# Kernel tuning notes

Measured on AMD Instinct MI355X. Metric: run time of the kernel, lower is better.

The kernel has to match this reference:

```python
import jax, jax.numpy as jnp
import numpy as np

D_MODEL = 1024
NUM_HEADS = 16
D_K = D_MODEL // NUM_HEADS


def setup_inputs() -> dict:
    key = jax.random.key(0)
    ks = jax.random.split(key, 11)
    s = 1.0 / np.sqrt(D_MODEL)
    return {
        "Q": jax.random.normal(ks[0], (2, 2048, D_MODEL), jnp.float32),
        "K": jax.random.normal(ks[1], (2, 2048, D_MODEL), jnp.float32),
        "V": jax.random.normal(ks[2], (2, 2048, D_MODEL), jnp.float32),
        "W_Q": jax.random.uniform(ks[3], (D_MODEL, D_MODEL), jnp.float32, -s, s),
        "b_Q": jax.random.uniform(ks[4], (D_MODEL,), jnp.float32, -s, s),
        "W_K": jax.random.uniform(ks[5], (D_K, D_MODEL), jnp.float32, -s, s),
        "b_K": jax.random.uniform(ks[6], (D_K,), jnp.float32, -s, s),
        "W_V": jax.random.uniform(ks[7], (D_K, D_MODEL), jnp.float32, -s, s),
        "b_V": jax.random.uniform(ks[8], (D_K,), jnp.float32, -s, s),
        "W_O": jax.random.uniform(ks[9], (D_MODEL, D_MODEL), jnp.float32, -s, s),
        "b_O": jax.random.uniform(ks[10], (D_MODEL,), jnp.float32, -s, s),
    }


def reference(Q, K, V, W_Q, b_Q, W_K, b_K, W_V, b_V, W_O, b_O):
    B, S, _ = Q.shape
    # Q projection -> [B, H, S, d_k]
    q = (Q @ W_Q.T + b_Q).reshape(B, S, NUM_HEADS, D_K).transpose(0, 2, 1, 3)
    # shared single-head K/V -> [B, S, d_k] (broadcast across heads)
    k = K @ W_K.T + b_K
    v = V @ W_V.T + b_V
    scale = 1.0 / jnp.sqrt(jnp.asarray(D_K, q.dtype))
    scores = jnp.einsum('bhqd,bkd->bhqk', q, k) * scale  # [B,H,S,S]
    attn = jax.nn.softmax(scores, axis=-1)
    out = jnp.einsum('bhqk,bkd->bhqd', attn, v)  # [B,H,S,d_k]
    out = out.transpose(0, 2, 1, 3).reshape(B, S, D_MODEL)
    return out @ W_O.T + b_O
```

## Files before the change

### kernel.cpp

```cpp
#include <hip/hip_runtime.h>
#include <hip/hip_bf16.h>
#include <math.h>

#define D_MODEL 1024
#define NUM_HEADS 16
#define DK 64
#define BATCH 2
#define SEQ 2048
#define MROWS (BATCH * SEQ)

#define QSCALE (0.125f * 1.4426950408889634f)

typedef __attribute__((ext_vector_type(8))) short bf16x8;
typedef __attribute__((ext_vector_type(4))) float f32x4;

static __device__ __forceinline__ short f2bf(float f) {
    __hip_bfloat16 h = __float2bfloat16(f);
    union { __hip_bfloat16 h; short s; } c; c.h = h; return c.s;
}

static __device__ __forceinline__ unsigned pkbf2(float a, float b) {
    __hip_bfloat162 h = __float22bfloat162_rn(make_float2(a, b));
    union { __hip_bfloat162 h; unsigned u; } c; c.h = h; return c.u;
}

static __device__ __forceinline__ void gload16(const void* g, void* l) {
    __builtin_amdgcn_global_load_lds(
        (const __attribute__((address_space(1))) unsigned int*)g,
        (__attribute__((address_space(3))) unsigned int*)l, 16, 0, 0);
}

__global__ __launch_bounds__(256) void cvt6(
    const float* __restrict__ q, const float* __restrict__ k,
    const float* __restrict__ v, const float* __restrict__ wq,
    const float* __restrict__ wo, const float* __restrict__ wk,
    const float* __restrict__ wv,
    short* __restrict__ qo, short* __restrict__ ko, short* __restrict__ vo,
    short* __restrict__ wqo, short* __restrict__ woo, short* __restrict__ wko,
    short* __restrict__ wvo)
{
    const int NB = (MROWS * D_MODEL) / 8;
    const int NW = (D_MODEL * D_MODEL) / 8;
    const int NS = (DK * D_MODEL) / 8;
    const int total = 3 * NB + 2 * NW + 2 * NS;
    for (int g = blockIdx.x * 256 + threadIdx.x; g < total; g += gridDim.x * 256) {
        const float* s; short* d; int x = g;
        if (x < NB)            { s = q;  d = qo;  }
        else if ((x -= NB) < NB) { s = k;  d = ko;  }
        else if ((x -= NB) < NB) { s = v;  d = vo;  }
        else if ((x -= NB) < NW) { s = wq; d = wqo; }
        else if ((x -= NW) < NW) { s = wo; d = woo; }
        else if ((x -= NW) < NS) { s = wk; d = wko; }
        else                     { x -= NS; s = wv; d = wvo; }
        float4 a = ((const float4*)s)[x * 2];
        float4 b = ((const float4*)s)[x * 2 + 1];
        uint4 hv;
        hv.x = pkbf2(a.x, a.y); hv.y = pkbf2(a.z, a.w);
        hv.z = pkbf2(b.x, b.y); hv.w = pkbf2(b.z, b.w);
        ((uint4*)d)[x] = hv;
    }
}

template<int MODE, int BM, int BN>
__global__ __launch_bounds__(256) void gemm97(
    const short* __restrict__ A, const short* __restrict__ W,
    const float* __restrict__ bias, void* __restrict__ Cp,
    const short* __restrict__ A2, const short* __restrict__ W2,
    const float* __restrict__ bias2, void* __restrict__ Cp2,
    int M, int N, int K, float outmult)
{
    constexpr int MI = BM / 32;
    constexpr int NI = BN / 32;
    constexpr int ACH = BM / 32;
    constexpr int WCH = BN / 32;
    __shared__ short As[BM * 64];
    __shared__ short Ws[BN * 64];

    int sel = 0;
    if (MODE == 2) {
        sel = blockIdx.y;
        if (sel) { A = A2; W = W2; bias = bias2; Cp = Cp2; }
    }
    const int bm = blockIdx.x * BM;
    const int bn = (MODE == 2) ? 0 : blockIdx.y * BN;
    const int tid = threadIdx.x;
    const int l = tid & 63, w = tid >> 6;
    const int lr = l & 15, lg = l >> 4;
    const int wm = (w >> 1) * (BM / 2), wn = (w & 1) * (BN / 2);

    f32x4 acc[MI][NI];
    #pragma unroll
    for (int mi = 0; mi < MI; mi++)
        #pragma unroll
        for (int ni = 0; ni < NI; ni++)
            acc[mi][ni] = (f32x4){0.f, 0.f, 0.f, 0.f};

    const int srow = l >> 3;
    const int scol = (l & 7) * 8;

    for (int k0 = 0; k0 < K; k0 += 64) {
        __syncthreads();
        #pragma unroll
        for (int i = 0; i < ACH; i++) {
            int c = w * ACH + i;
            gload16(A + (size_t)(bm + 8 * c + srow) * K + k0 + scol, As + c * 512);
        }
        #pragma unroll
        for (int i = 0; i < WCH; i++) {
            int c = w * WCH + i;
            gload16(W + (size_t)(bn + 8 * c + srow) * K + k0 + scol, Ws + c * 512);
        }
        __syncthreads();
        #pragma unroll
        for (int ks = 0; ks < 2; ks++) {
            bf16x8 af[MI], bf[NI];
            #pragma unroll
            for (int mi = 0; mi < MI; mi++)
                af[mi] = *(const bf16x8*)&As[(wm + mi * 16 + lr) * 64 + ks * 32 + 8 * lg];
            #pragma unroll
            for (int ni = 0; ni < NI; ni++)
                bf[ni] = *(const bf16x8*)&Ws[(wn + ni * 16 + lr) * 64 + ks * 32 + 8 * lg];
            #pragma unroll
            for (int mi = 0; mi < MI; mi++)
                #pragma unroll
                for (int ni = 0; ni < NI; ni++)
                    acc[mi][ni] = __builtin_amdgcn_mfma_f32_16x16x32_bf16(
                        af[mi], bf[ni], acc[mi][ni], 0, 0, 0);
        }
    }

    #pragma unroll
    for (int ni = 0; ni < NI; ni++) {
        int col = bn + wn + ni * 16 + lr;
        float bv = bias[col];
        #pragma unroll
        for (int mi = 0; mi < MI; mi++) {
            #pragma unroll
            for (int r = 0; r < 4; r++) {
                int row = bm + wm + mi * 16 + lg * 4 + r;
                float val = (acc[mi][ni][r] + bv) * outmult;
                if (MODE == 0) {
                    ((short*)Cp)[(size_t)row * N + col] = f2bf(val);
                } else if (MODE == 1) {
                    ((float*)Cp)[(size_t)row * N + col] = val;
                } else {
                    if (sel == 0) {
                        ((short*)Cp)[(size_t)row * DK + col] = f2bf(val);
                    } else {
                        int bi = row >> 11, si = row & (SEQ - 1);
                        int s6 = si & 63;
                        int sperm = (si & ~63) | (s6 & 32) |
                                    (((s6 >> 3) & 1) << 4) | (((s6 >> 2) & 1) << 3) |
                                    (((s6 >> 4) & 1) << 2) | (s6 & 3);
                        ((short*)Cp)[((size_t)bi * DK + col) * SEQ + sperm] = f2bf(val);
                    }
                }
            }
        }
    }
}

__global__ __launch_bounds__(128, 2) void mqa_attn_lds(
    const short* __restrict__ qb, const short* __restrict__ kb,
    const short* __restrict__ vt, short* __restrict__ ob)
{
    __shared__ char KsB[2][64 * 128];
    __shared__ char VsB[2][64 * 128];
    const int h = blockIdx.y, b = blockIdx.z;
    const int tid = threadIdx.x;
    const int l = tid & 63, w = tid >> 6;
    const int lr = l & 15, lg = l >> 4;
    const int q0 = blockIdx.x * 64 + w * 32;

    bf16x8 qf[2][2];
    #pragma unroll
    for (int qt = 0; qt < 2; qt++)
        #pragma unroll
        for (int kk = 0; kk < 2; kk++)
            qf[qt][kk] = *(const bf16x8*)(
                qb + (size_t)(b * SEQ + q0 + qt * 16 + lr) * D_MODEL + h * DK + kk * 32 + 8 * lg);

    int srow[4], scol[4];
    #pragma unroll
    for (int i = 0; i < 4; i++) {
        int s = i * 128 + w * 64 + l;
        srow[i] = s >> 3;
        int cb = (s & 7) * 16;
        scol[i] = (cb ^ ((srow[i] & 7) << 4)) >> 1;
    }

    f32x4 o[4][2];
    #pragma unroll
    for (int dt = 0; dt < 4; dt++)
        #pragma unroll
        for (int qt = 0; qt < 2; qt++)
            o[dt][qt] = (f32x4){0.f, 0.f, 0.f, 0.f};
    float m_i[2] = {-1e30f, -1e30f};
    float l_l[2] = {0.f, 0.f};

    #pragma unroll
    for (int i = 0; i < 4; i++) {
        gload16(kb + (size_t)(b * SEQ + 0 + srow[i]) * DK + scol[i],
                KsB[0] + (i * 128 + w * 64) * 16);
        gload16(vt + (size_t)(b * DK + srow[i]) * SEQ + 0 + scol[i],
                VsB[0] + (i * 128 + w * 64) * 16);
    }

    for (int t = 0; t < SEQ / 64; t++) {
        const int cur = t & 1;
        const int kt = t * 64;
        __syncthreads();
        if (t + 1 < SEQ / 64) {
            const int ktn = kt + 64;
            #pragma unroll
            for (int i = 0; i < 4; i++) {
                gload16(kb + (size_t)(b * SEQ + ktn + srow[i]) * DK + scol[i],
                        KsB[cur ^ 1] + (i * 128 + w * 64) * 16);
                gload16(vt + (size_t)(b * DK + srow[i]) * SEQ + ktn + scol[i],
                        VsB[cur ^ 1] + (i * 128 + w * 64) * 16);
            }
        }
        const char* Kc = KsB[cur];
        const char* Vc = VsB[cur];

        f32x4 s[2][4];
        #pragma unroll
        for (int qt = 0; qt < 2; qt++)
            #pragma unroll
            for (int j = 0; j < 4; j++) s[qt][j] = (f32x4){0.f, 0.f, 0.f, 0.f};
        #pragma unroll
        for (int kk = 0; kk < 2; kk++) {
            bf16x8 kf[4];
            #pragma unroll
            for (int j = 0; j < 4; j++) {
                int row = j * 16 + lr;
                kf[j] = *(const bf16x8*)(Kc + row * 128 + ((kk * 64 + 16 * lg) ^ ((row & 7) << 4)));
            }
            __builtin_amdgcn_s_setprio(1);
            #pragma unroll
            for (int qt = 0; qt < 2; qt++)
                #pragma unroll
                for (int j = 0; j < 4; j++)
                    s[qt][j] = __builtin_amdgcn_mfma_f32_16x16x32_bf16(
                        kf[j], qf[qt][kk], s[qt][j], 0, 0, 0);
            __builtin_amdgcn_s_setprio(0);
        }

        bf16x8 vf[2][4];
        #pragma unroll
        for (int kk = 0; kk < 2; kk++)
            #pragma unroll
            for (int dt = 0; dt < 4; dt++) {
                int row = dt * 16 + lr;
                vf[kk][dt] = *(const bf16x8*)(Vc + row * 128 + ((kk * 64 + 16 * lg) ^ ((row & 7) << 4)));
            }

        union { unsigned u[4]; bf16x8 v; } pku[2][2];
        #pragma unroll
        for (int qt = 0; qt < 2; qt++) {
            float mA = fmaxf(fmaxf(s[qt][0][0], s[qt][0][1]), s[qt][0][2]);
            float mB = fmaxf(fmaxf(s[qt][0][3], s[qt][1][0]), s[qt][1][1]);
            float mC = fmaxf(fmaxf(s[qt][1][2], s[qt][1][3]), s[qt][2][0]);
            float mD = fmaxf(fmaxf(s[qt][2][1], s[qt][2][2]), s[qt][2][3]);
            float mE = fmaxf(fmaxf(s[qt][3][0], s[qt][3][1]), s[qt][3][2]);
            float mx = fmaxf(fmaxf(fmaxf(mA, mB), mC),
                             fmaxf(fmaxf(mD, mE), s[qt][3][3]));

            if (__any(mx > m_i[qt] + 8.0f)) {
                float mxf = fmaxf(mx, __shfl_xor(mx, 16));
                mxf = fmaxf(mxf, __shfl_xor(mxf, 32));
                float mn = fmaxf(m_i[qt], mxf);
                float corr = __builtin_amdgcn_exp2f(m_i[qt] - mn);
                m_i[qt] = mn;
                l_l[qt] *= corr;
                #pragma unroll
                for (int dt = 0; dt < 4; dt++)
                    o[dt][qt] *= corr;
            }
            const float mnv = m_i[qt];

            float p[4][4];
            float rs = 0.f;
            #pragma unroll
            for (int j = 0; j < 4; j++) {
                p[j][0] = __builtin_amdgcn_exp2f(s[qt][j][0] - mnv);
                p[j][1] = __builtin_amdgcn_exp2f(s[qt][j][1] - mnv);
                p[j][2] = __builtin_amdgcn_exp2f(s[qt][j][2] - mnv);
                p[j][3] = __builtin_amdgcn_exp2f(s[qt][j][3] - mnv);
                rs += (p[j][0] + p[j][1]) + (p[j][2] + p[j][3]);
            }
            l_l[qt] += rs;

            pku[qt][0].u[0] = pkbf2(p[0][0], p[0][1]);
            pku[qt][0].u[1] = pkbf2(p[0][2], p[0][3]);
            pku[qt][0].u[2] = pkbf2(p[1][0], p[1][1]);
            pku[qt][0].u[3] = pkbf2(p[1][2], p[1][3]);
            pku[qt][1].u[0] = pkbf2(p[2][0], p[2][1]);
            pku[qt][1].u[1] = pkbf2(p[2][2], p[2][3]);
            pku[qt][1].u[2] = pkbf2(p[3][0], p[3][1]);
            pku[qt][1].u[3] = pkbf2(p[3][2], p[3][3]);
        }

        __builtin_amdgcn_s_setprio(1);
        #pragma unroll
        for (int kk = 0; kk < 2; kk++)
            #pragma unroll
            for (int dt = 0; dt < 4; dt++)
                #pragma unroll
                for (int qt = 0; qt < 2; qt++)
                    o[dt][qt] = __builtin_amdgcn_mfma_f32_16x16x32_bf16(
                        vf[kk][dt], pku[qt][kk].v, o[dt][qt], 0, 0, 0);
        __builtin_amdgcn_s_setprio(0);
    }

    #pragma unroll
    for (int qt = 0; qt < 2; qt++) {
        float lt = l_l[qt];
        lt += __shfl_xor(lt, 16);
        lt += __shfl_xor(lt, 32);
        float inv = 1.0f / lt;
        size_t grow = (size_t)(b * SEQ + q0 + qt * 16 + lr);
        #pragma unroll
        for (int dt = 0; dt < 4; dt++) {
            uint2 pk;
            pk.x = pkbf2(o[dt][qt][0] * inv, o[dt][qt][1] * inv);
            pk.y = pkbf2(o[dt][qt][2] * inv, o[dt][qt][3] * inv);
            *(uint2*)(ob + grow * D_MODEL + h * DK + dt * 16 + lg * 4) = pk;
        }
    }
}

extern "C" void kernel_launch(void* const* d_in, const int* in_sizes, int n_in,
                              void* d_out, int out_size, void* d_ws, size_t ws_size,
                              hipStream_t stream) {
    const float* Q   = (const float*)d_in[0];
    const float* K   = (const float*)d_in[1];
    const float* V   = (const float*)d_in[2];
    const float* W_Q = (const float*)d_in[3];
    const float* b_Q = (const float*)d_in[4];
    const float* W_K = (const float*)d_in[5];
    const float* b_K = (const float*)d_in[6];
    const float* W_V = (const float*)d_in[7];
    const float* b_V = (const float*)d_in[8];
    const float* W_O = (const float*)d_in[9];
    const float* b_O = (const float*)d_in[10];
    float* out = (float*)d_out;

    short* Qb  = (short*)d_ws;
    short* Kb  = Qb  + (size_t)MROWS * D_MODEL;
    short* Vb  = Kb  + (size_t)MROWS * D_MODEL;
    short* WQb = Vb  + (size_t)MROWS * D_MODEL;
    short* WKb = WQb + (size_t)D_MODEL * D_MODEL;
    short* WVb = WKb + (size_t)DK * D_MODEL;
    short* WOb = WVb + (size_t)DK * D_MODEL;
    short* qb  = WOb + (size_t)D_MODEL * D_MODEL;
    short* kb  = qb  + (size_t)MROWS * D_MODEL;
    short* vt  = kb  + (size_t)MROWS * DK;
    short* aws = vt  + (size_t)MROWS * DK;

    cvt6<<<2048, 256, 0, stream>>>(Q, K, V, W_Q, W_O, W_K, W_V,
                                   Qb, Kb, Vb, WQb, WOb, WKb, WVb);

    gemm97<0, 64, 128><<<dim3(MROWS / 64, D_MODEL / 128), 256, 0, stream>>>(
        Qb, WQb, b_Q, qb, nullptr, nullptr, nullptr, nullptr,
        MROWS, D_MODEL, D_MODEL, QSCALE);
    gemm97<2, 64, 64><<<dim3(MROWS / 64, 2), 256, 0, stream>>>(
        Kb, WKb, b_K, kb, Vb, WVb, b_V, vt, MROWS, DK, D_MODEL, 1.0f);
    mqa_attn_lds<<<dim3(SEQ / 64, NUM_HEADS, BATCH), 128, 0, stream>>>(
        qb, kb, vt, aws);
    gemm97<1, 64, 128><<<dim3(MROWS / 64, D_MODEL / 128), 256, 0, stream>>>(
        aws, WOb, b_O, out, nullptr, nullptr, nullptr, nullptr,
        MROWS, D_MODEL, D_MODEL, 1.0f);
}
```

Before: 131.3 us.

## Split KV tiles across wave pairs to overlap QK^T with softmax/PV, merge partials

The attention kernel now uses 256 threads: two wave pairs share each 64-query block, and each pair owns alternating KV tiles. In a given iteration one pair runs the QK^T MFMAs while the other runs softmax and PV on its earlier tile, so matrix and exponential work from different waves can overlap. At the end the two partial softmax states (max, sum, output) are merged through LDS. This adds an extra barrier per tile and an LDS combine step, and each wave keeps its score accumulators live across iterations, which raises register pressure.

Result: slower. 139.6 us (+6.4%).

```diff
diff --git a/kernel.cpp b/kernel.cpp
--- a/kernel.cpp
+++ b/kernel.cpp
@@ -160,17 +160,18 @@
     }
 }
 
-__global__ __launch_bounds__(128, 2) void mqa_attn_lds(
+__global__ __launch_bounds__(256, 4) void mqa_attn_pipe(
     const short* __restrict__ qb, const short* __restrict__ kb,
     const short* __restrict__ vt, short* __restrict__ ob)
 {
     __shared__ char KsB[2][64 * 128];
     __shared__ char VsB[2][64 * 128];
-    const int h = blockIdx.y, b = blockIdx.z;
+    const int hd = blockIdx.y, b = blockIdx.z;
     const int tid = threadIdx.x;
     const int l = tid & 63, w = tid >> 6;
+    const int qg = w >> 1, kp = w & 1;
     const int lr = l & 15, lg = l >> 4;
-    const int q0 = blockIdx.x * 64 + w * 32;
+    const int q0 = blockIdx.x * 64 + qg * 32;
 
     bf16x8 qf[2][2];
     #pragma unroll
@@ -178,12 +179,12 @@
         #pragma unroll
         for (int kk = 0; kk < 2; kk++)
             qf[qt][kk] = *(const bf16x8*)(
-                qb + (size_t)(b * SEQ + q0 + qt * 16 + lr) * D_MODEL + h * DK + kk * 32 + 8 * lg);
-
-    int srow[4], scol[4];
-    #pragma unroll
-    for (int i = 0; i < 4; i++) {
-        int s = i * 128 + w * 64 + l;
+                qb + (size_t)(b * SEQ + q0 + qt * 16 + lr) * D_MODEL + hd * DK + kk * 32 + 8 * lg);
+
+    int srow[2], scol[2];
+    #pragma unroll
+    for (int i = 0; i < 2; i++) {
+        int s = i * 256 + tid;
         srow[i] = s >> 3;
         int cb = (s & 7) * 16;
         scol[i] = (cb ^ ((srow[i] & 7) << 4)) >> 1;
@@ -197,75 +198,30 @@
             o[dt][qt] = (f32x4){0.f, 0.f, 0.f, 0.f};
     float m_i[2] = {-1e30f, -1e30f};
     float l_l[2] = {0.f, 0.f};
-
-    #pragma unroll
-    for (int i = 0; i < 4; i++) {
-        gload16(kb + (size_t)(b * SEQ + 0 + srow[i]) * DK + scol[i],
-                KsB[0] + (i * 128 + w * 64) * 16);
-        gload16(vt + (size_t)(b * DK + srow[i]) * SEQ + 0 + scol[i],
-                VsB[0] + (i * 128 + w * 64) * 16);
-    }
-
-    for (int t = 0; t < SEQ / 64; t++) {
-        const int cur = t & 1;
-        const int kt = t * 64;
-        __syncthreads();
-        if (t + 1 < SEQ / 64) {
-            const int ktn = kt + 64;
-            #pragma unroll
-            for (int i = 0; i < 4; i++) {
-                gload16(kb + (size_t)(b * SEQ + ktn + srow[i]) * DK + scol[i],
-                        KsB[cur ^ 1] + (i * 128 + w * 64) * 16);
-                gload16(vt + (size_t)(b * DK + srow[i]) * SEQ + ktn + scol[i],
-                        VsB[cur ^ 1] + (i * 128 + w * 64) * 16);
-            }
-        }
-        const char* Kc = KsB[cur];
-        const char* Vc = VsB[cur];
-
-        f32x4 s[2][4];
-        #pragma unroll
-        for (int qt = 0; qt < 2; qt++)
-            #pragma unroll
-            for (int j = 0; j < 4; j++) s[qt][j] = (f32x4){0.f, 0.f, 0.f, 0.f};
-        #pragma unroll
-        for (int kk = 0; kk < 2; kk++) {
-            bf16x8 kf[4];
-            #pragma unroll
-            for (int j = 0; j < 4; j++) {
-                int row = j * 16 + lr;
-                kf[j] = *(const bf16x8*)(Kc + row * 128 + ((kk * 64 + 16 * lg) ^ ((row & 7) << 4)));
-            }
-            __builtin_amdgcn_s_setprio(1);
-            #pragma unroll
-            for (int qt = 0; qt < 2; qt++)
-                #pragma unroll
-                for (int j = 0; j < 4; j++)
-                    s[qt][j] = __builtin_amdgcn_mfma_f32_16x16x32_bf16(
-                        kf[j], qf[qt][kk], s[qt][j], 0, 0, 0);
-            __builtin_amdgcn_s_setprio(0);
-        }
-
-        bf16x8 vf[2][4];
-        #pragma unroll
-        for (int kk = 0; kk < 2; kk++)
-            #pragma unroll
-            for (int dt = 0; dt < 4; dt++) {
-                int row = dt * 16 + lr;
-                vf[kk][dt] = *(const bf16x8*)(Vc + row * 128 + ((kk * 64 + 16 * lg) ^ ((row & 7) << 4)));
-            }
-
-        union { unsigned u[4]; bf16x8 v; } pku[2][2];
+    f32x4 sS[2][4];
+
+    #pragma unroll
+    for (int i = 0; i < 2; i++) {
+        gload16(kb + (size_t)(b * SEQ + srow[i]) * DK + scol[i],
+                KsB[0] + (i * 256 + tid) * 16);
+        gload16(vt + (size_t)(b * DK + srow[i]) * SEQ + scol[i],
+                VsB[0] + (i * 256 + tid) * 16);
+    }
+
+    const char* Kc = KsB[kp];
+    const char* Vc = VsB[kp];
+
+    auto finishTile = [&]() {
+        union PKU { unsigned u[4]; bf16x8 v; } pku[2][2];
         #pragma unroll
         for (int qt = 0; qt < 2; qt++) {
-            float mA = fmaxf(fmaxf(s[qt][0][0], s[qt][0][1]), s[qt][0][2]);
-            float mB = fmaxf(fmaxf(s[qt][0][3], s[qt][1][0]), s[qt][1][1]);
-            float mC = fmaxf(fmaxf(s[qt][1][2], s[qt][1][3]), s[qt][2][0]);
-            float mD = fmaxf(fmaxf(s[qt][2][1], s[qt][2][2]), s[qt][2][3]);
-            float mE = fmaxf(fmaxf(s[qt][3][0], s[qt][3][1]), s[qt][3][2]);
+            float mA = fmaxf(fmaxf(sS[qt][0][0], sS[qt][0][1]), sS[qt][0][2]);
+            float mB = fmaxf(fmaxf(sS[qt][0][3], sS[qt][1][0]), sS[qt][1][1]);
+            float mC = fmaxf(fmaxf(sS[qt][1][2], sS[qt][1][3]), sS[qt][2][0]);
+            float mD = fmaxf(fmaxf(sS[qt][2][1], sS[qt][2][2]), sS[qt][2][3]);
+            float mE = fmaxf(fmaxf(sS[qt][3][0], sS[qt][3][1]), sS[qt][3][2]);
             float mx = fmaxf(fmaxf(fmaxf(mA, mB), mC),
-                             fmaxf(fmaxf(mD, mE), s[qt][3][3]));
-
+                             fmaxf(fmaxf(mD, mE), sS[qt][3][3]));
             if (__any(mx > m_i[qt] + 8.0f)) {
                 float mxf = fmaxf(mx, __shfl_xor(mx, 16));
                 mxf = fmaxf(mxf, __shfl_xor(mxf, 32));
@@ -278,19 +234,17 @@
                     o[dt][qt] *= corr;
             }
             const float mnv = m_i[qt];
-
             float p[4][4];
             float rs = 0.f;
             #pragma unroll
             for (int j = 0; j < 4; j++) {
-                p[j][0] = __builtin_amdgcn_exp2f(s[qt][j][0] - mnv);
-                p[j][1] = __builtin_amdgcn_exp2f(s[qt][j][1] - mnv);
-                p[j][2] = __builtin_amdgcn_exp2f(s[qt][j][2] - mnv);
-                p[j][3] = __builtin_amdgcn_exp2f(s[qt][j][3] - mnv);
+                p[j][0] = __builtin_amdgcn_exp2f(sS[qt][j][0] - mnv);
+                p[j][1] = __builtin_amdgcn_exp2f(sS[qt][j][1] - mnv);
+                p[j][2] = __builtin_amdgcn_exp2f(sS[qt][j][2] - mnv);
+                p[j][3] = __builtin_amdgcn_exp2f(sS[qt][j][3] - mnv);
                 rs += (p[j][0] + p[j][1]) + (p[j][2] + p[j][3]);
             }
             l_l[qt] += rs;
-
             pku[qt][0].u[0] = pkbf2(p[0][0], p[0][1]);
             pku[qt][0].u[1] = pkbf2(p[0][2], p[0][3]);
             pku[qt][0].u[2] = pkbf2(p[1][0], p[1][1]);
@@ -300,32 +254,114 @@
             pku[qt][1].u[2] = pkbf2(p[3][0], p[3][1]);
             pku[qt][1].u[3] = pkbf2(p[3][2], p[3][3]);
         }
-
-        __builtin_amdgcn_s_setprio(1);
-        #pragma unroll
-        for (int kk = 0; kk < 2; kk++)
+        #pragma unroll
+        for (int kk = 0; kk < 2; kk++) {
+            bf16x8 vfk[4];
+            #pragma unroll
+            for (int dt = 0; dt < 4; dt++) {
+                int row = dt * 16 + lr;
+                vfk[dt] = *(const bf16x8*)(Vc + row * 128 + ((kk * 64 + 16 * lg) ^ ((row & 7) << 4)));
+            }
+            __builtin_amdgcn_s_setprio(1);
             #pragma unroll
             for (int dt = 0; dt < 4; dt++)
                 #pragma unroll
                 for (int qt = 0; qt < 2; qt++)
                     o[dt][qt] = __builtin_amdgcn_mfma_f32_16x16x32_bf16(
-                        vf[kk][dt], pku[qt][kk].v, o[dt][qt], 0, 0, 0);
-        __builtin_amdgcn_s_setprio(0);
-    }
-
+                        vfk[dt], pku[qt][kk].v, o[dt][qt], 0, 0, 0);
+            __builtin_amdgcn_s_setprio(0);
+        }
+    };
+
+    for (int t = 0; t < SEQ / 64; t++) {
+        __syncthreads();
+        if ((t & 1) == kp) {
+            #pragma unroll
+            for (int qt = 0; qt < 2; qt++)
+                #pragma unroll
+                for (int j = 0; j < 4; j++) sS[qt][j] = (f32x4){0.f, 0.f, 0.f, 0.f};
+            #pragma unroll
+            for (int kk = 0; kk < 2; kk++) {
+                bf16x8 kf[4];
+                #pragma unroll
+                for (int j = 0; j < 4; j++) {
+                    int row = j * 16 + lr;
+                    kf[j] = *(const bf16x8*)(Kc + row * 128 + ((kk * 64 + 16 * lg) ^ ((row & 7) << 4)));
+                }
+                __builtin_amdgcn_s_setprio(1);
+                #pragma unroll
+                for (int qt = 0; qt < 2; qt++)
+                    #pragma unroll
+                    for (int j = 0; j < 4; j++)
+                        sS[qt][j] = __builtin_amdgcn_mfma_f32_16x16x32_bf16(
+                            kf[j], qf[qt][kk], sS[qt][j], 0, 0, 0);
+                __builtin_amdgcn_s_setprio(0);
+            }
+        } else if (t > 0) {
+            finishTile();
+        }
+        __syncthreads();
+        if (t + 1 < SEQ / 64) {
+            const int ktn = (t + 1) * 64;
+            char* Kd = KsB[(t + 1) & 1];
+            char* Vd = VsB[(t + 1) & 1];
+            #pragma unroll
+            for (int i = 0; i < 2; i++) {
+                gload16(kb + (size_t)(b * SEQ + ktn + srow[i]) * DK + scol[i],
+                        Kd + (i * 256 + tid) * 16);
+                gload16(vt + (size_t)(b * DK + srow[i]) * SEQ + ktn + scol[i],
+                        Vd + (i * 256 + tid) * 16);
+            }
+        }
+    }
+    if (kp == 1) finishTile();
+
+    float lw[2];
     #pragma unroll
     for (int qt = 0; qt < 2; qt++) {
-        float lt = l_l[qt];
-        lt += __shfl_xor(lt, 16);
-        lt += __shfl_xor(lt, 32);
-        float inv = 1.0f / lt;
-        size_t grow = (size_t)(b * SEQ + q0 + qt * 16 + lr);
-        #pragma unroll
-        for (int dt = 0; dt < 4; dt++) {
-            uint2 pk;
-            pk.x = pkbf2(o[dt][qt][0] * inv, o[dt][qt][1] * inv);
-            pk.y = pkbf2(o[dt][qt][2] * inv, o[dt][qt][3] * inv);
-            *(uint2*)(ob + grow * D_MODEL + h * DK + dt * 16 + lg * 4) = pk;
+        float x = l_l[qt];
+        x += __shfl_xor(x, 16);
+        x += __shfl_xor(x, 32);
+        lw[qt] = x;
+    }
+    if (kp == 1) {
+        float* ml = (float*)VsB[0];
+        char* OS = (char*)KsB;
+        #pragma unroll
+        for (int qt = 0; qt < 2; qt++) {
+            ml[((qg * 2 + qt) * 2 + 0) * 16 + lr] = m_i[qt];
+            ml[((qg * 2 + qt) * 2 + 1) * 16 + lr] = lw[qt];
+            #pragma unroll
+            for (int dt = 0; dt < 4; dt++)
+                *(f32x4*)(OS + qg * 8192 + (qt * 16 + lr) * 256 +
+                          ((dt * 64 + lg * 16) ^ ((lr & 7) << 4))) = o[dt][qt];
+        }
+    }
+    __syncthreads();
+    if (kp == 0) {
+        const float* ml = (const float*)VsB[0];
+        const char* OS = (const char*)KsB;
+        #pragma unroll
+        for (int qt = 0; qt < 2; qt++) {
+            float m1 = ml[((qg * 2 + qt) * 2 + 0) * 16 + lr];
+            float l1 = ml[((qg * 2 + qt) * 2 + 1) * 16 + lr];
+            float mM = fmaxf(m_i[qt], m1);
+            float c0 = __builtin_amdgcn_exp2f(m_i[qt] - mM);
+            float c1 = __builtin_amdgcn_exp2f(m1 - mM);
+            float inv = 1.0f / (lw[qt] * c0 + l1 * c1);
+            float a0 = c0 * inv, a1 = c1 * inv;
+            size_t grow = (size_t)(b * SEQ + q0 + qt * 16 + lr);
+            #pragma unroll
+            for (int dt = 0; dt < 4; dt++) {
+                f32x4 ov = *(const f32x4*)(OS + qg * 8192 + (qt * 16 + lr) * 256 +
+                                           ((dt * 64 + lg * 16) ^ ((lr & 7) << 4)));
+                uint2 pk;
+                pk.x = pkbf2(o[dt][qt][0] * a0 + ov[0] * a1,
+                             o[dt][qt][1] * a0 + ov[1] * a1);
+                pk.y = pkbf2(o[dt][qt][2] * a0 + ov[2] * a1,
+                             o[dt][qt][3] * a0 + ov[3] * a1);
+                *(uint2*)(ob + grow * D_MODEL + hd * DK + dt * 16 + lg * 4) = pk;
+            }
         }
     }
 }
@@ -366,7 +402,7 @@
         MROWS, D_MODEL, D_MODEL, QSCALE);
     gemm97<2, 64, 64><<<dim3(MROWS / 64, 2), 256, 0, stream>>>(
         Kb, WKb, b_K, kb, Vb, WVb, b_V, vt, MROWS, DK, D_MODEL, 1.0f);
-    mqa_attn_lds<<<dim3(SEQ / 64, NUM_HEADS, BATCH), 128, 0, stream>>>(
+    mqa_attn_pipe<<<dim3(SEQ / 64, NUM_HEADS, BATCH), 256, 0, stream>>>(
         qb, kb, vt, aws);
     gemm97<1, 64, 128><<<dim3(MROWS / 64, D_MODEL / 128), 256, 0, stream>>>(
         aws, WOb, b_O, out, nullptr, nullptr, nullptr, nullptr,
```
